# Kernel optimization log

Hardware: AMD Instinct MI355X
Metric: run time of the kernel (lower is better)

The kernel has to match this reference:

```python
import jax, jax.numpy as jnp
import numpy as np

B, C, L = 16, 256, 2048

def setup_inputs() -> dict:
    key = jax.random.key(0)
    k1, k2, k3, k4 = jax.random.split(key, 4)
    return {
        "proj_query": jax.random.normal(k1, (B, C, L), dtype=jnp.float32),
        "proj_key": jax.random.normal(k2, (B, C, L), dtype=jnp.float32),
        "proj_val": jax.random.normal(k3, (B, C, L), dtype=jnp.float32),
        "padding_mask": jax.random.uniform(k4, (B, 1, L), dtype=jnp.float32),
    }

def reference(proj_query, proj_key, proj_val, padding_mask):
    c = proj_query.shape[1]
    # energy[b,l,m] = sum_c Q[b,c,l] * K[b,c,m]  -> (B, L, L)
    energy = jnp.einsum("bcl,bcm->blm", proj_query, proj_key) / jnp.sqrt(jnp.float32(c))
    # log-additive padding mask (the tril mask in the source is dead code, never applied)
    logits = energy + jnp.log(padding_mask + 1e-9)
    attention = jax.nn.softmax(logits, axis=-1)
    # post-softmax multiplicative mask
    attention = attention * padding_mask
    # out[b,c,l] = sum_m V[b,c,m] * attention[b,l,m]  -> (B, C, L)
    out = jnp.einsum("bcm,blm->bcl", proj_val, attention)
    return out
```

## Files before the change

kernel.cpp:

```cpp
#include <hip/hip_runtime.h>
#include <hip/hip_bf16.h>

#define B_ 16
#define C_ 256
#define L_ 2048
#define MT 32

typedef __attribute__((ext_vector_type(8))) short bf16x8;
typedef __attribute__((ext_vector_type(4))) float f32x4;

#define CEXP 0.09016844005556021f

__device__ __forceinline__ short f2bf_rne(float f) {
    union { float f; unsigned u; } x; x.f = f;
    unsigned r = x.u + 0x7fffu + ((x.u >> 16) & 1u);
    return (short)(r >> 16);
}

__device__ __forceinline__ void gld_lds16(const void* g, void* l) {
    __builtin_amdgcn_global_load_lds(
        (const __attribute__((address_space(1))) void*)g,
        (__attribute__((address_space(3))) void*)l, 16, 0, 0);
}

__device__ __forceinline__ void barrier_lds_only() {
    asm volatile("" ::: "memory");
    __builtin_amdgcn_s_waitcnt(0xC07F);
    __builtin_amdgcn_s_barrier();
    asm volatile("" ::: "memory");
}

__global__ __launch_bounds__(256) void prepass_kernel(
        const float* __restrict__ Kin, const float* __restrict__ Vin,
        const float* __restrict__ mask,
        short* __restrict__ Kt, short* __restrict__ Vb) {
    const int bid = blockIdx.x;
    const int t = threadIdx.x;
    if (bid < 512) {
        __shared__ unsigned short tile[64 * 256];
        const int b  = bid >> 5;
        const int l0 = (bid & 31) * 64;
        #pragma unroll
        for (int iter = 0; iter < 16; ++iter) {
            int idx = iter * 256 + t;
            int ci = idx >> 4;
            int lc = (idx & 15) * 4;
            float4 v = *(const float4*)(Kin + ((size_t)(b * C_ + ci)) * L_ + l0 + lc);
            float vv[4] = {v.x, v.y, v.z, v.w};
            #pragma unroll
            for (int j = 0; j < 4; ++j) {
                int l = lc + j;
                tile[l * 256 + (((ci >> 3) ^ (l & 31)) << 3) + (ci & 7)] =
                    (unsigned short)f2bf_rne(vv[j]);
            }
        }
        __syncthreads();
        #pragma unroll
        for (int iter = 0; iter < 8; ++iter) {
            int li = iter * 8 + (t >> 5);
            int ck = t & 31;
            uint4 val = *(const uint4*)(tile + li * 256 + ((ck ^ (li & 31)) << 3));
            *(uint4*)(Kt + ((size_t)(b * L_ + l0 + li)) * C_ + ck * 8) = val;
        }
    } else {
        size_t e = ((size_t)(bid - 512) * 256 + t) * 8;
        int b = (int)(e >> 19);
        int m = (int)(e & (L_ - 1));
        const float4 v0 = *(const float4*)(Vin + e);
        const float4 v1 = *(const float4*)(Vin + e + 4);
        const float* mp = mask + ((size_t)b << 11) + m;
        const float4 m0 = *(const float4*)mp;
        const float4 m1 = *(const float4*)(mp + 4);
        uint4 o;
        o.x = (unsigned)(unsigned short)f2bf_rne(v0.x * m0.x)
            | ((unsigned)(unsigned short)f2bf_rne(v0.y * m0.y) << 16);
        o.y = (unsigned)(unsigned short)f2bf_rne(v0.z * m0.z)
            | ((unsigned)(unsigned short)f2bf_rne(v0.w * m0.w) << 16);
        o.z = (unsigned)(unsigned short)f2bf_rne(v1.x * m1.x)
            | ((unsigned)(unsigned short)f2bf_rne(v1.y * m1.y) << 16);
        o.w = (unsigned)(unsigned short)f2bf_rne(v1.z * m1.z)
            | ((unsigned)(unsigned short)f2bf_rne(v1.w * m1.w) << 16);
        *(uint4*)(Vb + e) = o;
    }
}

__device__ __forceinline__ void stage_K(const short* __restrict__ Ksrc,
                                        short* Ks, int m0, int t) {
    #pragma unroll
    for (int rr = 0; rr < 4; ++rr) {
        int G = rr * 256 + t;
        int m = G >> 5, p = G & 31;
        gld_lds16(Ksrc + ((size_t)(m0 + m) << 8) + ((p ^ m) << 3), Ks + G * 8);
    }
}

__device__ __forceinline__ void load_V(bf16x8 (&vf)[4], const short* __restrict__ Vw, int m0) {
    #pragma unroll
    for (int ct = 0; ct < 4; ++ct)
        vf[ct] = *(const bf16x8*)(Vw + (size_t)(ct * 16) * L_ + m0);
}

#define ATTN_ITER(KS_CUR, KS_NXT, VF_CUR, VF_NXT, M0, GUARD)                               \
  {                                                                                        \
    __syncthreads();                   \
    if (!(GUARD) || ((M0) + MT < L_)) {                                                    \
      stage_K(Ksrc, KS_NXT, (M0) + MT, t);                                                 \
      load_V(VF_NXT, Vw, (M0) + MT);                                                       \
    }                                                                                      \
    float wv = mrow[(M0) + 16 * mt + n] + 1e-9f;                                           \
    f32x4 S0 = fzero, S1 = fzero;                                                          \
    const short* Krow = KS_CUR + (16 * mt + n) * 256;                                      \
    _Pragma("unroll")                                                                      \
    for (int ks = 0; ks < 8; ++ks) {                                                       \
      bf16x8 bf = *(const bf16x8*)(Krow + (((4 * ks + q) ^ (16 * mt + n)) << 3));          \
      S0 = __builtin_amdgcn_mfma_f32_16x16x32_bf16(qf[0][ks], bf, S0, 0, 0, 0);            \
      S1 = __builtin_amdgcn_mfma_f32_16x16x32_bf16(qf[1][ks], bf, S1, 0, 0, 0);            \
    }                                                                                      \
    _Pragma("unroll")                                                                      \
    for (int r = 0; r < 4; ++r) {                                                          \
      float p0 = wv * exp2f(S0[r]);                                                        \
      dn[0][r] += p0;                                                                      \
      Pw0[(4 * r) * 40] = f2bf_rne(p0);                                                    \
      float p1 = wv * exp2f(S1[r]);                                                        \
      dn[1][r] += p1;                                                                      \
      Pw0[(16 + 4 * r) * 40] = f2bf_rne(p1);                                               \
    }                                                                                      \
    barrier_lds_only();                     \
    bf16x8 af[4];                                                                          \
    _Pragma("unroll")                                                                      \
    for (int lt = 0; lt < 4; ++lt)                                                         \
      af[lt] = *(const bf16x8*)(Pl + (16 * lt + 4 * (n & 3) + (n >> 2)) * 40 + 8 * q);     \
    _Pragma("unroll")                                                                      \
    for (int ct = 0; ct < 4; ++ct)                                                         \
      _Pragma("unroll")                                                                    \
      for (int lt = 0; lt < 4; ++lt)                                                       \
        Oacc[lt][ct] =                                                                     \
            __builtin_amdgcn_mfma_f32_16x16x32_bf16(af[lt], VF_CUR[ct], Oacc[lt][ct], 0, 0, 0); \
  }

__global__ __launch_bounds__(256, 2) void attn_main(
        const float* __restrict__ Qin,
        const short* __restrict__ Kt,
        const short* __restrict__ Vb,
        const float* __restrict__ mask,
        float* __restrict__ out) {
    __shared__ __align__(16) char smem[38400];
    short* KsB0 = (short*)smem;
    short* KsB1 = (short*)(smem + 16384);
    short* Pl   = (short*)(smem + 32768);
    float* Dsh  = (float*)(smem + 37888);

    const int t = threadIdx.x;
    const int w = t >> 6, lane = t & 63, q = lane >> 4, n = lane & 15;
    const int g = w & 1, mt = w >> 1;

    const int b  = blockIdx.x & 15;
    const int l0 = (blockIdx.x >> 4) * 64;

    const short* Ksrc = Kt + (size_t)b * (L_ * C_);
    const short* Vsrc = Vb + (size_t)b * (C_ * L_);
    const float* mrow = mask + (size_t)b * L_;
    const short* Vw   = Vsrc + (size_t)(64 * w + n) * L_ + 8 * q;
    short* Pw0 = Pl + (32 * g + q) * 40 + 16 * mt + n;

    bf16x8 qf[2][8];
    {
        const float* Qb = Qin + (size_t)b * (C_ * L_) + (l0 + 32 * g + n);
        #pragma unroll
        for (int lt = 0; lt < 2; ++lt)
            #pragma unroll
            for (int ks = 0; ks < 8; ++ks) {
                bf16x8 v;
                #pragma unroll
                for (int j = 0; j < 8; ++j) {
                    float f = Qb[(size_t)(32 * ks + 8 * q + j) * L_ + 16 * lt];
                    v[j] = f2bf_rne(f * CEXP);
                }
                qf[lt][ks] = v;
            }
    }

    const f32x4 fzero = {0.f, 0.f, 0.f, 0.f};
    f32x4 Oacc[4][4];
    #pragma unroll
    for (int i = 0; i < 4; ++i)
        #pragma unroll
        for (int j = 0; j < 4; ++j) Oacc[i][j] = fzero;
    float dn[2][4] = {{0.f,0.f,0.f,0.f},{0.f,0.f,0.f,0.f}};

    stage_K(Ksrc, KsB0, 0, t);
    bf16x8 vfA[4], vfB[4];
    load_V(vfA, Vw, 0);

    #pragma unroll 1
    for (int it2 = 0; it2 < L_ / MT / 2; ++it2) {
        const int m0 = it2 * (2 * MT);
        ATTN_ITER(KsB0, KsB1, vfA, vfB, m0, false)
        ATTN_ITER(KsB1, KsB0, vfB, vfA, m0 + MT, true)
    }

    #pragma unroll
    for (int d = 1; d < 16; d <<= 1) {
        #pragma unroll
        for (int lt = 0; lt < 2; ++lt)
            #pragma unroll
            for (int r = 0; r < 4; ++r)
                dn[lt][r] += __shfl_xor(dn[lt][r], d, 64);
    }
    __syncthreads();
    if (n == 0) {
        #pragma unroll
        for (int lt = 0; lt < 2; ++lt)
            #pragma unroll
            for (int r = 0; r < 4; ++r)
                Dsh[mt * 64 + 32 * g + 16 * lt + 4 * q + r] = dn[lt][r];
    }
    __syncthreads();

    float rden[4][4];
    #pragma unroll
    for (int lt = 0; lt < 4; ++lt)
        #pragma unroll
        for (int r = 0; r < 4; ++r) {
            int l = 16 * lt + 4 * q + r;
            rden[lt][r] = 1.0f / (Dsh[l] + Dsh[64 + l]);
        }

    float* ob = out + (size_t)b * (C_ * L_) + l0;
    #pragma unroll
    for (int lt = 0; lt < 4; ++lt)
        #pragma unroll
        for (int ct = 0; ct < 4; ++ct) {
            int c = 64 * w + 16 * ct + n;
            float4 val;
            val.x = Oacc[lt][ct][0] * rden[lt][0];
            val.y = Oacc[lt][ct][1] * rden[lt][1];
            val.z = Oacc[lt][ct][2] * rden[lt][2];
            val.w = Oacc[lt][ct][3] * rden[lt][3];
            *(float4*)(ob + (size_t)c * L_ + 16 * lt + 4 * q) = val;
        }
}

extern "C" void kernel_launch(void* const* d_in, const int* in_sizes, int n_in,
                              void* d_out, int out_size, void* d_ws, size_t ws_size,
                              hipStream_t stream) {
    const float* Q    = (const float*)d_in[0];
    const float* K    = (const float*)d_in[1];
    const float* V    = (const float*)d_in[2];
    const float* mask = (const float*)d_in[3];
    float* out = (float*)d_out;

    short* Kt = (short*)d_ws;
    short* Vb = Kt + (size_t)B_ * L_ * C_;

    prepass_kernel<<<4608, 256, 0, stream>>>(K, V, mask, Kt, Vb);
    attn_main<<<512, 256, 0, stream>>>(Q, Kt, Vb, mask, out);
}
```

Before: 237.3 us.

## Double-buffer P tile and software-pipeline PV MFMA with next QK tile

Splits the per-tile attention step into an S phase (QK^T, exp, write P to LDS) and an O phase (read P, multiply by V). P now uses two LDS buffers, so the O phase of the previous tile runs after the same barrier as the S phase of the current tile. This drops one of the two block barriers per tile and lets the two MFMA streams interleave. In exchange, LDS use grows by about 5 KB, register pressure rises slightly, and a final O phase is added after the loop.

```diff
diff --git a/kernel.cpp b/kernel.cpp
--- a/kernel.cpp
+++ b/kernel.cpp
@@ -21,13 +21,6 @@
     __builtin_amdgcn_global_load_lds(
         (const __attribute__((address_space(1))) void*)g,
         (__attribute__((address_space(3))) void*)l, 16, 0, 0);
-}
-
-__device__ __forceinline__ void barrier_lds_only() {
-    asm volatile("" ::: "memory");
-    __builtin_amdgcn_s_waitcnt(0xC07F);
-    __builtin_amdgcn_s_barrier();
-    asm volatile("" ::: "memory");
 }
 
 __global__ __launch_bounds__(256) void prepass_kernel(
@@ -100,16 +93,24 @@
         vf[ct] = *(const bf16x8*)(Vw + (size_t)(ct * 16) * L_ + m0);
 }
 
-#define ATTN_ITER(KS_CUR, KS_NXT, VF_CUR, VF_NXT, M0, GUARD)                               \
+#define O_PHASE(PBUF, VF)                                                                  \
   {                                                                                        \
-    __syncthreads();                   \
-    if (!(GUARD) || ((M0) + MT < L_)) {                                                    \
-      stage_K(Ksrc, KS_NXT, (M0) + MT, t);                                                 \
-      load_V(VF_NXT, Vw, (M0) + MT);                                                       \
-    }                                                                                      \
-    float wv = mrow[(M0) + 16 * mt + n] + 1e-9f;                                           \
+    bf16x8 af[4];                                                                          \
+    _Pragma("unroll")                                                                      \
+    for (int lt = 0; lt < 4; ++lt)                                                         \
+      af[lt] = *(const bf16x8*)((PBUF) + (16 * lt + 4 * (n & 3) + (n >> 2)) * 40 + 8 * q); \
+    _Pragma("unroll")                                                                      \
+    for (int ct = 0; ct < 4; ++ct)                                                         \
+      _Pragma("unroll")                                                                    \
+      for (int lt = 0; lt < 4; ++lt)                                                       \
+        Oacc[lt][ct] =                                                                     \
+            __builtin_amdgcn_mfma_f32_16x16x32_bf16(af[lt], (VF)[ct], Oacc[lt][ct], 0, 0, 0); \
+  }
+
+#define S_PHASE(KS, PW0)                                                                   \
+  {                                                                                        \
     f32x4 S0 = fzero, S1 = fzero;                                                          \
-    const short* Krow = KS_CUR + (16 * mt + n) * 256;                                      \
+    const short* Krow = (KS) + (16 * mt + n) * 256;                                        \
     _Pragma("unroll")                                                                      \
     for (int ks = 0; ks < 8; ++ks) {                                                       \
       bf16x8 bf = *(const bf16x8*)(Krow + (((4 * ks + q) ^ (16 * mt + n)) << 3));          \
@@ -120,22 +121,11 @@
     for (int r = 0; r < 4; ++r) {                                                          \
       float p0 = wv * exp2f(S0[r]);                                                        \
       dn[0][r] += p0;                                                                      \
-      Pw0[(4 * r) * 40] = f2bf_rne(p0);                                                    \
+      (PW0)[(4 * r) * 40] = f2bf_rne(p0);                                                  \
       float p1 = wv * exp2f(S1[r]);                                                        \
       dn[1][r] += p1;                                                                      \
-      Pw0[(16 + 4 * r) * 40] = f2bf_rne(p1);                                               \
+      (PW0)[(16 + 4 * r) * 40] = f2bf_rne(p1);                                             \
     }                                                                                      \
-    barrier_lds_only();                     \
-    bf16x8 af[4];                                                                          \
-    _Pragma("unroll")                                                                      \
-    for (int lt = 0; lt < 4; ++lt)                                                         \
-      af[lt] = *(const bf16x8*)(Pl + (16 * lt + 4 * (n & 3) + (n >> 2)) * 40 + 8 * q);     \
-    _Pragma("unroll")                                                                      \
-    for (int ct = 0; ct < 4; ++ct)                                                         \
-      _Pragma("unroll")                                                                    \
-      for (int lt = 0; lt < 4; ++lt)                                                       \
-        Oacc[lt][ct] =                                                                     \
-            __builtin_amdgcn_mfma_f32_16x16x32_bf16(af[lt], VF_CUR[ct], Oacc[lt][ct], 0, 0, 0); \
   }
 
 __global__ __launch_bounds__(256, 2) void attn_main(
@@ -144,11 +134,12 @@
         const short* __restrict__ Vb,
         const float* __restrict__ mask,
         float* __restrict__ out) {
-    __shared__ __align__(16) char smem[38400];
+    __shared__ __align__(16) char smem[43520];
     short* KsB0 = (short*)smem;
     short* KsB1 = (short*)(smem + 16384);
-    short* Pl   = (short*)(smem + 32768);
-    float* Dsh  = (float*)(smem + 37888);
+    short* PA   = (short*)(smem + 32768);
+    short* PB   = (short*)(smem + 37888);
+    float* Dsh  = (float*)(smem + 43008);
 
     const int t = threadIdx.x;
     const int w = t >> 6, lane = t & 63, q = lane >> 4, n = lane & 15;
@@ -161,7 +152,8 @@
     const short* Vsrc = Vb + (size_t)b * (C_ * L_);
     const float* mrow = mask + (size_t)b * L_;
     const short* Vw   = Vsrc + (size_t)(64 * w + n) * L_ + 8 * q;
-    short* Pw0 = Pl + (32 * g + q) * 40 + 16 * mt + n;
+    short* Pw0A = PA + (32 * g + q) * 40 + 16 * mt + n;
+    short* Pw0B = PB + (32 * g + q) * 40 + 16 * mt + n;
 
     bf16x8 qf[2][8];
     {
@@ -191,13 +183,35 @@
     stage_K(Ksrc, KsB0, 0, t);
     bf16x8 vfA[4], vfB[4];
     load_V(vfA, Vw, 0);
+    float wv = mrow[16 * mt + n] + 1e-9f;
 
     #pragma unroll 1
     for (int it2 = 0; it2 < L_ / MT / 2; ++it2) {
-        const int m0 = it2 * (2 * MT);
-        ATTN_ITER(KsB0, KsB1, vfA, vfB, m0, false)
-        ATTN_ITER(KsB1, KsB0, vfB, vfA, m0 + MT, true)
-    }
+        const int m0a = it2 * (2 * MT);
+        const int m0b = m0a + MT;
+
+        __syncthreads();
+        if (m0a != 0) O_PHASE(PB, vfB)
+        stage_K(Ksrc, KsB1, m0a + MT, t);
+        load_V(vfB, Vw, m0a + MT);
+        float wvn0 = mrow[m0a + MT + 16 * mt + n] + 1e-9f;
+        S_PHASE(KsB0, Pw0A)
+        wv = wvn0;
+
+        __syncthreads();
+        O_PHASE(PA, vfA)
+        float wvn1 = 0.f;
+        if (m0b + MT < L_) {
+            stage_K(Ksrc, KsB0, m0b + MT, t);
+            load_V(vfA, Vw, m0b + MT);
+            wvn1 = mrow[m0b + MT + 16 * mt + n] + 1e-9f;
+        }
+        S_PHASE(KsB1, Pw0B)
+        wv = wvn1;
+    }
+
+    __syncthreads();
+    O_PHASE(PB, vfB)
 
     #pragma unroll
     for (int d = 1; d < 16; d <<= 1) {
@@ -207,7 +221,6 @@
             for (int r = 0; r < 4; ++r)
                 dn[lt][r] += __shfl_xor(dn[lt][r], d, 64);
     }
-    __syncthreads();
     if (n == 0) {
         #pragma unroll
         for (int lt = 0; lt < 2; ++lt)
```

Result: faster. 230.7 us (-2.8%).
